# Optimization experiments

Hardware: AMD Instinct MI355X
Metric: run time of the kernel (lower is better)

## Reference

```python
import jax, jax.numpy as jnp
import numpy as np

N, C, D, V, NC = 60000, 4, 200, 5000, 250


def _lin(key, out_d, in_d):
    # torch nn.Linear default init: U(-1/sqrt(in), 1/sqrt(in))
    s = 1.0 / np.sqrt(in_d)
    k1, k2 = jax.random.split(key)
    w = jax.random.uniform(k1, (out_d, in_d), minval=-s, maxval=s, dtype=jnp.float32)
    b = jax.random.uniform(k2, (out_d,), minval=-s, maxval=s, dtype=jnp.float32)
    return w, b


def setup_inputs() -> dict:
    key = jax.random.key(0)
    ks = jax.random.split(key, 16)
    inp = {}
    inp['tokens'] = jax.random.randint(ks[0], (N,), 0, V)
    inp['child_c'] = jax.random.normal(ks[1], (N, C, D), dtype=jnp.float32)
    inp['child_h'] = jax.random.normal(ks[2], (N, C, D), dtype=jnp.float32)
    inp['emb'] = jax.random.normal(ks[3], (V, D), dtype=jnp.float32)
    # ForBlock: proj1: 3D->D, proj2: 2D->D
    inp['p1_w'], inp['p1_b'] = _lin(ks[4], D, 3 * D)
    inp['p2_w'], inp['p2_b'] = _lin(ks[5], D, 2 * D)
    # treelstm gates (each Linear D->D)
    for i, g in enumerate(['ix', 'ih', 'fx', 'fh', 'ux', 'uh', 'ox', 'oh']):
        w, b = _lin(ks[6 + i], D, D)
        inp[g + '_w'], inp[g + '_b'] = w, b
    inp['fc2_w'], inp['fc2_b'] = _lin(ks[14], NC, D)
    return inp


def reference(tokens, child_c, child_h, emb,
              p1_w, p1_b, p2_w, p2_b,
              ix_w, ix_b, ih_w, ih_b, fx_w, fx_b, fh_w, fh_b,
              ux_w, ux_b, uh_w, uh_b, ox_w, ox_b, oh_w, oh_b,
              fc2_w, fc2_b):
    x = emb[tokens]  # [N, D] node token embeddings (nn.Embedding lookup)
    # ForBlock: control = relu(proj1(cat[init, cond, next])); hsum = relu(proj2(cat[control, block]))
    control = jax.nn.relu(
        jnp.concatenate([child_h[:, 0], child_h[:, 1], child_h[:, 2]], axis=-1) @ p1_w.T + p1_b)
    child_h_sum = jax.nn.relu(
        jnp.concatenate([control, child_h[:, 3]], axis=-1) @ p2_w.T + p2_b)  # [N, D]
    # treelstm.node update (vectorized over N nodes, C children)
    i = jax.nn.sigmoid(x @ ix_w.T + ix_b + child_h_sum @ ih_w.T + ih_b)
    o = jax.nn.sigmoid(x @ ox_w.T + ox_b + child_h_sum @ oh_w.T + oh_b)
    u = jnp.tanh(x @ ux_w.T + ux_b + child_h_sum @ uh_w.T + uh_b)
    fx = (x @ fx_w.T + fx_b)[:, None, :]  # [N, 1, D]
    f = jax.nn.sigmoid(jnp.einsum('ncd,md->ncm', child_h, fh_w) + fh_b + fx)  # [N, C, D]
    c = i * u + jnp.sum(f * child_c, axis=1)  # [N, D]
    h = o * jnp.tanh(c)  # [N, D]
    logits = h @ fc2_w.T + fc2_b  # [N, n_class]
    return logits
```

## Files before the change

kernel.cpp:

```cpp
#include <hip/hip_runtime.h>
#include <cmath>

#define NNODES 60000
#define DDIM   200
#define NCLS   250

constexpr int R   = 64;
constexpr int BK  = 32;
constexpr int XP  = 232;

typedef float  f32x4  __attribute__((ext_vector_type(4)));
typedef short  short8 __attribute__((ext_vector_type(8)));

constexpr int W_P1  = 0;
constexpr int W_P2A = 155648;
constexpr int W_P2B = 212992;
constexpr int W_FX  = 270336;
constexpr int W_FH  = 327680;
constexpr int W_IX  = 385024;
constexpr int W_IH  = 442368;
constexpr int W_UX  = 499712;
constexpr int W_UH  = 557056;
constexpr int W_OX  = 614400;
constexpr int W_OH  = 671744;
constexpr int W_FC2 = 729088;
constexpr int W_TOTAL_ELEMS = 786432;
constexpr size_t W_TOTAL_BYTES = (size_t)W_TOTAL_ELEMS * 2;

__device__ __forceinline__ short f2b(float f) {
    union { float f; unsigned u; } x; x.f = f;
    unsigned r = (x.u + 0x7FFFu + ((x.u >> 16) & 1u)) >> 16;
    return (short)r;
}
__device__ __forceinline__ float b2f(short s) {
    union { unsigned u; float f; } x; x.u = ((unsigned)(unsigned short)s) << 16;
    return x.f;
}
__device__ __forceinline__ float sgm(float x)  { return 1.0f / (1.0f + __expf(-x)); }
__device__ __forceinline__ float tanh_fast(float x) { return 1.0f - 2.0f / (__expf(2.0f * x) + 1.0f); }
__device__ __forceinline__ int   swz(int b)    { return b ^ (((b >> 7) & 3) << 4); }

__global__ void wprep(const float* __restrict__ p1w, const float* __restrict__ p2w,
                      const float* __restrict__ fxw, const float* __restrict__ fhw,
                      const float* __restrict__ ixw, const float* __restrict__ ihw,
                      const float* __restrict__ uxw, const float* __restrict__ uhw,
                      const float* __restrict__ oxw, const float* __restrict__ ohw,
                      const float* __restrict__ fc2w, short* __restrict__ ws)
{
    int i = blockIdx.x * 256 + threadIdx.x;
    if (i >= W_TOTAL_ELEMS) return;
    float v = 0.0f;
    if (i < W_P2A) {
        int n = i / 608, k = i % 608;
        if (n < 200 && k < 600) v = p1w[n * 600 + k];
        ws[i] = f2b(v); return;
    }
    int j = i - W_P2A;
    int m = j / 57344, rem = j % 57344;
    int n = rem / 224, k = rem % 224;
    const float* src; int stride = 200, off = 0, ncols = 200;
    switch (m) {
        case 0:  src = p2w; stride = 400; break;
        case 1:  src = p2w; stride = 400; off = 200; break;
        case 2:  src = fxw; break;
        case 3:  src = fhw; break;
        case 4:  src = ixw; break;
        case 5:  src = ihw; break;
        case 6:  src = uxw; break;
        case 7:  src = uhw; break;
        case 8:  src = oxw; break;
        case 9:  src = ohw; break;
        default: src = fc2w; ncols = 250; break;
    }
    if (n < ncols && k < 200) v = src[n * stride + off + k];
    ws[i] = f2b(v);
}

__device__ __forceinline__ void gload16(const void* g, void* l) {
    __builtin_amdgcn_global_load_lds((const __attribute__((address_space(1))) unsigned*)g,
                                     (__attribute__((address_space(3))) unsigned*)l, 16, 0, 0);
}

__device__ __forceinline__ void stage_w(const short* __restrict__ wmat, int Kpad, int t,
                                        int wrows, int wv, short* w_sw)
{
    const int issues = wrows >> 4;
    for (int q = wv; q < issues; q += 4) {
        const int lane = threadIdx.x & 63;
        const int db = q * 1024 + lane * 16;
        const int n  = db >> 6;
        const int g  = (db >> 4) & 3;
        const int gs = g ^ ((n >> 1) & 3);
        const short* src = wmat + (long)n * Kpad + t * BK + gs * 8;
        char* dst = ((char*)w_sw) + q * 1024;
        gload16(src, dst);
    }
}

__device__ __forceinline__ void stage_a_chh(short* a_sw, const float* __restrict__ ag,
                                            int row0, int colofs, int k0, int Kreal, int tid)
{
    const int r = tid >> 2, gq = tid & 3;
    long rg = row0 + r; if (rg >= NNODES) rg = NNODES - 1;
    const float* src = ag + rg * 800 + colofs + k0 + gq * 8;
    short8 v;
    if (k0 + BK <= Kreal) {
        float4 f0 = *(const float4*)(src);
        float4 f1 = *(const float4*)(src + 4);
        v[0] = f2b(f0.x); v[1] = f2b(f0.y); v[2] = f2b(f0.z); v[3] = f2b(f0.w);
        v[4] = f2b(f1.x); v[5] = f2b(f1.y); v[6] = f2b(f1.z); v[7] = f2b(f1.w);
    } else {
        #pragma unroll
        for (int i = 0; i < 8; ++i) {
            int k = k0 + gq * 8 + i;
            float f = (k < Kreal) ? src[i] : 0.0f;
            v[i] = f2b(f);
        }
    }
    int b = r * 64 + gq * 16; b = swz(b);
    *(short8*)((char*)a_sw + b) = v;
}

template<int NF, bool FROM_GLOBAL>
__device__ __forceinline__ void gemm_pass(
    f32x4 (*acc)[8],
    const short (*Ap)[XP],
    const float* __restrict__ ag, int row0, int colofs, int Kreal,
    const short* __restrict__ wmat, int ktiles, int Kpad, int wrows,
    short* a_sw, short* w_sw,
    int tid, int wv, int wm, int wn, int l15, int lg)
{
    for (int t = 0; t < ktiles; ++t) {
        __syncthreads();
        stage_w(wmat, Kpad, t, wrows, wv, w_sw);
        if constexpr (FROM_GLOBAL)
            stage_a_chh(a_sw, ag, row0, colofs, t * BK, Kreal, tid);
        __syncthreads();
        short8 af[2];
        #pragma unroll
        for (int mi = 0; mi < 2; ++mi) {
            const int row = wm * 32 + mi * 16 + l15;
            if constexpr (FROM_GLOBAL) {
                int b = swz(row * 64 + lg * 16);
                af[mi] = *(const short8*)((const char*)a_sw + b);
            } else {
                af[mi] = *(const short8*)&Ap[row][t * BK + lg * 8];
            }
        }
        #pragma unroll
        for (int ni = 0; ni < NF; ++ni) {
            const int n = (wn * NF + ni) * 16 + l15;
            int b = swz(n * 64 + lg * 16);
            short8 bf = *(const short8*)((const char*)w_sw + b);
            #pragma unroll
            for (int mi = 0; mi < 2; ++mi)
                acc[mi][ni] = __builtin_amdgcn_mfma_f32_16x16x32_bf16(af[mi], bf, acc[mi][ni], 0, 0, 0);
        }
    }
}

#define ZERO_ACC()  { _Pragma("unroll") for (int mi_=0; mi_<2; ++mi_) { _Pragma("unroll") for (int ni_=0; ni_<8; ++ni_) { _Pragma("unroll") for (int q_=0;q_<4;++q_) acc[mi_][ni_][q_] = 0.0f; } } }

__global__ __launch_bounds__(256, 2)
void fused_mfma(const int* __restrict__ tok,
                const float* __restrict__ chc,
                const float* __restrict__ chh,
                const float* __restrict__ emb,
                const float* __restrict__ p1b_, const float* __restrict__ p2b_,
                const float* __restrict__ ixb, const float* __restrict__ ihb,
                const float* __restrict__ fxb, const float* __restrict__ fhb,
                const float* __restrict__ uxb, const float* __restrict__ uhb,
                const float* __restrict__ oxb, const float* __restrict__ ohb,
                const float* __restrict__ fc2b,
                const short* __restrict__ ws,
                float* __restrict__ out)
{
    __shared__ __align__(16) short x_lds[R][XP];
    __shared__ __align__(16) short hbuf[R][XP];
    __shared__ __align__(16) short a_sw[R * BK];
    __shared__ __align__(16) short w_sw[8192];

    const int tid = threadIdx.x;
    const int wv = tid >> 6, wm = wv >> 1, wn = wv & 1;
    const int l15 = tid & 15, lg = (tid & 63) >> 4;
    const int row0 = blockIdx.x * R;

    {
        const int r = tid >> 2, q = tid & 3;
        #pragma unroll
        for (int c = 200 + q * 8; c < 200 + q * 8 + 8; ++c) { x_lds[r][c] = 0; hbuf[r][c] = 0; }
        long rg = row0 + r; if (rg >= NNODES) rg = NNODES - 1;
        const float* er = emb + (long)tok[rg] * DDIM;
        const int c0 = q * 50;
        #pragma unroll
        for (int i = 0; i < 50; i += 2) {
            float2 f = *(const float2*)(er + c0 + i);
            x_lds[r][c0 + i]     = f2b(f.x);
            x_lds[r][c0 + i + 1] = f2b(f.y);
        }
    }

    f32x4 acc[2][8];

    ZERO_ACC();
    gemm_pass<7, true>(acc, nullptr, chh, row0, 0, 600, ws + W_P1, 19, 608, 224,
                       a_sw, w_sw, tid, wv, wm, wn, l15, lg);
    #pragma unroll
    for (int mi = 0; mi < 2; ++mi)
        #pragma unroll
        for (int ni = 0; ni < 7; ++ni) {
            const int col = (wn * 7 + ni) * 16 + l15;
            if (col < DDIM) {
                const float b = p1b_[col];
                #pragma unroll
                for (int j = 0; j < 4; ++j) {
                    const int lrow = wm * 32 + mi * 16 + lg * 4 + j;
                    hbuf[lrow][col] = f2b(fmaxf(acc[mi][ni][j] + b, 0.0f));
                }
            }
        }

    ZERO_ACC();
    gemm_pass<7, false>(acc, hbuf, nullptr, 0, 0, 0, ws + W_P2A, 7, 224, 224,
                        a_sw, w_sw, tid, wv, wm, wn, l15, lg);
    gemm_pass<7, true>(acc, nullptr, chh, row0, 600, 200, ws + W_P2B, 7, 224, 224,
                       a_sw, w_sw, tid, wv, wm, wn, l15, lg);
    #pragma unroll
    for (int mi = 0; mi < 2; ++mi)
        #pragma unroll
        for (int ni = 0; ni < 7; ++ni) {
            const int col = (wn * 7 + ni) * 16 + l15;
            if (col < DDIM) {
                const float b = p2b_[col];
                #pragma unroll
                for (int j = 0; j < 4; ++j) {
                    const int lrow = wm * 32 + mi * 16 + lg * 4 + j;
                    hbuf[lrow][col] = f2b(fmaxf(acc[mi][ni][j] + b, 0.0f));
                }
            }
        }

    float giu[2][7][4];
    ZERO_ACC();
    gemm_pass<7, false>(acc, x_lds, nullptr, 0, 0, 0, ws + W_IX, 7, 224, 224,
                        a_sw, w_sw, tid, wv, wm, wn, l15, lg);
    gemm_pass<7, false>(acc, hbuf, nullptr, 0, 0, 0, ws + W_IH, 7, 224, 224,
                        a_sw, w_sw, tid, wv, wm, wn, l15, lg);
    #pragma unroll
    for (int mi = 0; mi < 2; ++mi)
        #pragma unroll
        for (int ni = 0; ni < 7; ++ni) {
            const int col = (wn * 7 + ni) * 16 + l15;
            const float b = (col < DDIM) ? (ixb[col] + ihb[col]) : 0.0f;
            #pragma unroll
            for (int j = 0; j < 4; ++j) giu[mi][ni][j] = sgm(acc[mi][ni][j] + b);
        }

    ZERO_ACC();
    gemm_pass<7, false>(acc, x_lds, nullptr, 0, 0, 0, ws + W_UX, 7, 224, 224,
                        a_sw, w_sw, tid, wv, wm, wn, l15, lg);
    gemm_pass<7, false>(acc, hbuf, nullptr, 0, 0, 0, ws + W_UH, 7, 224, 224,
                        a_sw, w_sw, tid, wv, wm, wn, l15, lg);
    #pragma unroll
    for (int mi = 0; mi < 2; ++mi)
        #pragma unroll
        for (int ni = 0; ni < 7; ++ni) {
            const int col = (wn * 7 + ni) * 16 + l15;
            const float b = (col < DDIM) ? (uxb[col] + uhb[col]) : 0.0f;
            #pragma unroll
            for (int j = 0; j < 4; ++j) giu[mi][ni][j] *= tanh_fast(acc[mi][ni][j] + b);
        }

    ZERO_ACC();
    gemm_pass<7, false>(acc, x_lds, nullptr, 0, 0, 0, ws + W_OX, 7, 224, 224,
                        a_sw, w_sw, tid, wv, wm, wn, l15, lg);
    gemm_pass<7, false>(acc, hbuf, nullptr, 0, 0, 0, ws + W_OH, 7, 224, 224,
                        a_sw, w_sw, tid, wv, wm, wn, l15, lg);
    __syncthreads();
    #pragma unroll
    for (int mi = 0; mi < 2; ++mi)
        #pragma unroll
        for (int ni = 0; ni < 7; ++ni) {
            const int col = (wn * 7 + ni) * 16 + l15;
            if (col < DDIM) {
                const float b = oxb[col] + ohb[col];
                #pragma unroll
                for (int j = 0; j < 4; ++j) {
                    const int lrow = wm * 32 + mi * 16 + lg * 4 + j;
                    hbuf[lrow][col] = f2b(sgm(acc[mi][ni][j] + b));
                }
            }
        }

    float fxr[2][7][4];
    ZERO_ACC();
    gemm_pass<7, false>(acc, x_lds, nullptr, 0, 0, 0, ws + W_FX, 7, 224, 224,
                        a_sw, w_sw, tid, wv, wm, wn, l15, lg);
    #pragma unroll
    for (int mi = 0; mi < 2; ++mi)
        #pragma unroll
        for (int ni = 0; ni < 7; ++ni) {
            const int col = (wn * 7 + ni) * 16 + l15;
            const float b = (col < DDIM) ? fxb[col] : 0.0f;
            #pragma unroll
            for (int j = 0; j < 4; ++j) fxr[mi][ni][j] = acc[mi][ni][j] + b;
        }

    __syncthreads();
    #pragma unroll
    for (int mi = 0; mi < 2; ++mi)
        #pragma unroll
        for (int ni = 0; ni < 7; ++ni) {
            const int col = (wn * 7 + ni) * 16 + l15;
            if (col < DDIM) {
                #pragma unroll
                for (int j = 0; j < 4; ++j) {
                    const int lrow = wm * 32 + mi * 16 + lg * 4 + j;
                    x_lds[lrow][col] = f2b(giu[mi][ni][j]);
                }
            }
        }

    float csum[2][7][4];
    #pragma unroll
    for (int mi = 0; mi < 2; ++mi)
        #pragma unroll
        for (int ni = 0; ni < 7; ++ni)
            #pragma unroll
            for (int j = 0; j < 4; ++j) csum[mi][ni][j] = 0.0f;

    for (int c = 0; c < 4; ++c) {
        ZERO_ACC();
        gemm_pass<7, true>(acc, nullptr, chh, row0, c * 200, 200, ws + W_FH, 7, 224, 224,
                           a_sw, w_sw, tid, wv, wm, wn, l15, lg);
        #pragma unroll
        for (int mi = 0; mi < 2; ++mi)
            #pragma unroll
            for (int ni = 0; ni < 7; ++ni) {
                const int col = (wn * 7 + ni) * 16 + l15;
                if (col < DDIM) {
                    const float b = fhb[col];
                    #pragma unroll
                    for (int j = 0; j < 4; ++j) {
                        const int lrow = wm * 32 + mi * 16 + lg * 4 + j;
                        long rg = row0 + lrow; if (rg >= NNODES) rg = NNODES - 1;
                        const float cv = chc[rg * 800 + c * 200 + col];
                        csum[mi][ni][j] += sgm(acc[mi][ni][j] + b + fxr[mi][ni][j]) * cv;
                    }
                }
            }
    }

    #pragma unroll
    for (int mi = 0; mi < 2; ++mi)
        #pragma unroll
        for (int ni = 0; ni < 7; ++ni) {
            const int col = (wn * 7 + ni) * 16 + l15;
            if (col < DDIM) {
                #pragma unroll
                for (int j = 0; j < 4; ++j) {
                    const int lrow = wm * 32 + mi * 16 + lg * 4 + j;
                    const float iu = b2f(x_lds[lrow][col]);
                    const float o  = b2f(hbuf[lrow][col]);
                    const float cc = iu + csum[mi][ni][j];
                    hbuf[lrow][col] = f2b(o * tanh_fast(cc));
                }
            }
        }

    ZERO_ACC();
    gemm_pass<8, false>(acc, hbuf, nullptr, 0, 0, 0, ws + W_FC2, 7, 224, 256,
                        a_sw, w_sw, tid, wv, wm, wn, l15, lg);
    #pragma unroll
    for (int mi = 0; mi < 2; ++mi)
        #pragma unroll
        for (int ni = 0; ni < 8; ++ni) {
            const int col = (wn * 8 + ni) * 16 + l15;
            if (col < NCLS) {
                const float b = fc2b[col];
                #pragma unroll
                for (int j = 0; j < 4; ++j) {
                    const int lrow = wm * 32 + mi * 16 + lg * 4 + j;
                    const long gr = row0 + lrow;
                    if (gr < NNODES) out[gr * NCLS + col] = acc[mi][ni][j] + b;
                }
            }
        }
}

constexpr int FRT = 32, FBK = 16, FNT = 256, FRTP = FRT + 4, FBUFP = 208;
__device__ __forceinline__ float sgm_f(float x) { return 1.0f / (1.0f + expf(-x)); }

__device__ __forceinline__ void f_stage(
    float (*aT)[FRTP], float (*wt)[FNT], int row0, int k0,
    const float* a1g, int a1pitch, const int* gidx, const float* a1l, int a1lp, int K1,
    const float* a2g, int a2pitch, const float* a2l, int a2lp, int K2,
    const float* wa, int wap, int KW1, const float* wb, int wbp,
    int ncols, int tid)
{
    const int Ktot = K1 + K2;
    {
        const int kk = tid & 15, k = k0 + kk;
        #pragma unroll
        for (int h = 0; h < 2; ++h) {
            const int r = (tid >> 4) + h * 16;
            float v = 0.0f;
            if (k < K1) {
                if (a1l) v = a1l[r * a1lp + k];
                else {
                    const long rb = gidx ? (long)gidx[row0 + r] * a1pitch : (long)(row0 + r) * a1pitch;
                    v = a1g[rb + k];
                }
            } else if (k < Ktot) {
                if (a2l) v = a2l[r * a2lp + (k - K1)];
                else     v = a2g[(long)(row0 + r) * a2pitch + (k - K1)];
            }
            aT[kk][r] = v;
        }
    }
    {
        const int col = tid;
        #pragma unroll
        for (int kk = 0; kk < FBK; ++kk) {
            const int k = k0 + kk; float v = 0.0f;
            if (col < ncols && k < Ktot) {
                if (k < KW1) v = wa[(long)col * wap + k];
                else         v = wb[(long)col * wbp + (k - KW1)];
            }
            wt[kk][col] = v;
        }
    }
}
__device__ __forceinline__ void f_gemm(
    float (*aT)[FRTP], float (*wt)[FNT], float acc[8][4], int row0,
    const float* a1g, int a1p, const int* gidx, const float* a1l, int a1lp, int K1,
    const float* a2g, int a2p, const float* a2l, int a2lp, int K2,
    const float* wa, int wap, int KW1, const float* wb, int wbp,
    int ncols, int tid, int tr, int tc)
{
    #pragma unroll
    for (int j = 0; j < 8; ++j)
        #pragma unroll
        for (int i = 0; i < 4; ++i) acc[j][i] = 0.0f;
    const int Ktot = K1 + K2;
    for (int k0 = 0; k0 < Ktot; k0 += FBK) {
        __syncthreads();
        f_stage(aT, wt, row0, k0, a1g, a1p, gidx, a1l, a1lp, K1, a2g, a2p, a2l, a2lp, K2,
                wa, wap, KW1, wb, wbp, ncols, tid);
        __syncthreads();
        #pragma unroll
        for (int kk = 0; kk < FBK; ++kk) {
            const float w0 = wt[kk][tc*4+0], w1 = wt[kk][tc*4+1], w2 = wt[kk][tc*4+2], w3 = wt[kk][tc*4+3];
            #pragma unroll
            for (int j = 0; j < 8; ++j) {
                const float a = aT[kk][tr*8+j];
                acc[j][0] = fmaf(a, w0, acc[j][0]); acc[j][1] = fmaf(a, w1, acc[j][1]);
                acc[j][2] = fmaf(a, w2, acc[j][2]); acc[j][3] = fmaf(a, w3, acc[j][3]);
            }
        }
    }
}
__global__ __launch_bounds__(256)
void fused_fp32(const int* tok, const float* chc, const float* chh, const float* emb,
                const float* p1w, const float* p1b, const float* p2w, const float* p2b,
                const float* ixw, const float* ixb, const float* ihw, const float* ihb,
                const float* fxw, const float* fxb, const float* fhw, const float* fhb,
                const float* uxw, const float* uxb, const float* uhw, const float* uhb,
                const float* oxw, const float* oxb, const float* ohw, const float* ohb,
                const float* fc2w, const float* fc2b, float* out)
{
    __shared__ float aT[FBK][FRTP]; __shared__ float wt[FBK][FNT]; __shared__ float buf[FRT][FBUFP];
    const int tid = threadIdx.x, tr = tid >> 6, tc = tid & 63, c0 = tc * 4;
    const int row0 = blockIdx.x * FRT;
    float acc[8][4];
    f_gemm(aT, wt, acc, row0, chh, 800, nullptr, nullptr, 0, 600, nullptr,0,nullptr,0,0, p1w,600,600,nullptr,0, DDIM, tid,tr,tc);
    if (c0 < DDIM) { const float4 b = *(const float4*)&p1b[c0];
        #pragma unroll
        for (int j=0;j<8;++j){int r=tr*8+j; buf[r][c0]=fmaxf(acc[j][0]+b.x,0.f); buf[r][c0+1]=fmaxf(acc[j][1]+b.y,0.f); buf[r][c0+2]=fmaxf(acc[j][2]+b.z,0.f); buf[r][c0+3]=fmaxf(acc[j][3]+b.w,0.f);} }
    f_gemm(aT, wt, acc, row0, nullptr,0,nullptr,&buf[0][0],FBUFP,200, chh+600,800,nullptr,0,200, p2w,400,400,nullptr,0, DDIM, tid,tr,tc);
    if (c0 < DDIM) { const float4 b = *(const float4*)&p2b[c0];
        #pragma unroll
        for (int j=0;j<8;++j){int r=tr*8+j; buf[r][c0]=fmaxf(acc[j][0]+b.x,0.f); buf[r][c0+1]=fmaxf(acc[j][1]+b.y,0.f); buf[r][c0+2]=fmaxf(acc[j][2]+b.z,0.f); buf[r][c0+3]=fmaxf(acc[j][3]+b.w,0.f);} }
    f_gemm(aT, wt, acc, row0, emb, DDIM, tok, nullptr,0,200, nullptr,0,nullptr,0,0, fxw,200,200,nullptr,0, DDIM, tid,tr,tc);
    float fxr[8][4];
    { float4 b = make_float4(0,0,0,0); if (c0<DDIM) b = *(const float4*)&fxb[c0];
      #pragma unroll
      for (int j=0;j<8;++j){fxr[j][0]=acc[j][0]+b.x;fxr[j][1]=acc[j][1]+b.y;fxr[j][2]=acc[j][2]+b.z;fxr[j][3]=acc[j][3]+b.w;} }
    float csum[8][4];
    #pragma unroll
    for (int j=0;j<8;++j)
        #pragma unroll
        for (int i=0;i<4;++i) csum[j][i]=0.f;
    for (int cc_=0; cc_<4; ++cc_) {
        f_gemm(aT, wt, acc, row0, chh+cc_*200,800,nullptr,nullptr,0,200, nullptr,0,nullptr,0,0, fhw,200,200,nullptr,0, DDIM, tid,tr,tc);
        if (c0 < DDIM) { const float4 b = *(const float4*)&fhb[c0];
            #pragma unroll
            for (int j=0;j<8;++j){ const long r=row0+tr*8+j; const float4 cv=*(const float4*)&chc[r*800+cc_*200+c0];
                csum[j][0]+=sgm_f(acc[j][0]+b.x+fxr[j][0])*cv.x; csum[j][1]+=sgm_f(acc[j][1]+b.y+fxr[j][1])*cv.y;
                csum[j][2]+=sgm_f(acc[j][2]+b.z+fxr[j][2])*cv.z; csum[j][3]+=sgm_f(acc[j][3]+b.w+fxr[j][3])*cv.w; } }
    }
    f_gemm(aT, wt, acc, row0, emb, DDIM, tok, nullptr,0,200, nullptr,0,&buf[0][0],FBUFP,200, ixw,200,200,ihw,200, DDIM, tid,tr,tc);
    float gi[8][4];
    { float4 b1=make_float4(0,0,0,0),b2=b1; if(c0<DDIM){b1=*(const float4*)&ixb[c0];b2=*(const float4*)&ihb[c0];}
      #pragma unroll
      for(int j=0;j<8;++j){gi[j][0]=sgm_f(acc[j][0]+b1.x+b2.x);gi[j][1]=sgm_f(acc[j][1]+b1.y+b2.y);gi[j][2]=sgm_f(acc[j][2]+b1.z+b2.z);gi[j][3]=sgm_f(acc[j][3]+b1.w+b2.w);} }
    f_gemm(aT, wt, acc, row0, emb, DDIM, tok, nullptr,0,200, nullptr,0,&buf[0][0],FBUFP,200, uxw,200,200,uhw,200, DDIM, tid,tr,tc);
    float cval[8][4];
    { float4 b1=make_float4(0,0,0,0),b2=b1; if(c0<DDIM){b1=*(const float4*)&uxb[c0];b2=*(const float4*)&uhb[c0];}
      #pragma unroll
      for(int j=0;j<8;++j){cval[j][0]=gi[j][0]*tanhf(acc[j][0]+b1.x+b2.x)+csum[j][0];cval[j][1]=gi[j][1]*tanhf(acc[j][1]+b1.y+b2.y)+csum[j][1];
                           cval[j][2]=gi[j][2]*tanhf(acc[j][2]+b1.z+b2.z)+csum[j][2];cval[j][3]=gi[j][3]*tanhf(acc[j][3]+b1.w+b2.w)+csum[j][3];} }
    f_gemm(aT, wt, acc, row0, emb, DDIM, tok, nullptr,0,200, nullptr,0,&buf[0][0],FBUFP,200, oxw,200,200,ohw,200, DDIM, tid,tr,tc);
    if (c0 < DDIM) { const float4 b1=*(const float4*)&oxb[c0], b2=*(const float4*)&ohb[c0];
        #pragma unroll
        for(int j=0;j<8;++j){int r=tr*8+j;
            buf[r][c0]=sgm_f(acc[j][0]+b1.x+b2.x)*tanhf(cval[j][0]); buf[r][c0+1]=sgm_f(acc[j][1]+b1.y+b2.y)*tanhf(cval[j][1]);
            buf[r][c0+2]=sgm_f(acc[j][2]+b1.z+b2.z)*tanhf(cval[j][2]); buf[r][c0+3]=sgm_f(acc[j][3]+b1.w+b2.w)*tanhf(cval[j][3]);} }
    f_gemm(aT, wt, acc, row0, nullptr,0,nullptr,&buf[0][0],FBUFP,200, nullptr,0,nullptr,0,0, fc2w,200,200,nullptr,0, NCLS, tid,tr,tc);
    #pragma unroll
    for (int j=0;j<8;++j){ const long r=row0+tr*8+j;
        #pragma unroll
        for (int i=0;i<4;++i){ const int col=c0+i; if (col<NCLS) out[r*NCLS+col]=acc[j][i]+fc2b[col]; } }
}

extern "C" void kernel_launch(void* const* d_in, const int* in_sizes, int n_in,
                              void* d_out, int out_size, void* d_ws, size_t ws_size,
                              hipStream_t stream)
{
    const int*   tok  = (const int*)  d_in[0];
    const float* chc  = (const float*)d_in[1];
    const float* chh  = (const float*)d_in[2];
    const float* emb  = (const float*)d_in[3];
    const float* p1w  = (const float*)d_in[4];
    const float* p1b  = (const float*)d_in[5];
    const float* p2w  = (const float*)d_in[6];
    const float* p2b  = (const float*)d_in[7];
    const float* ixw  = (const float*)d_in[8];
    const float* ixb  = (const float*)d_in[9];
    const float* ihw  = (const float*)d_in[10];
    const float* ihb  = (const float*)d_in[11];
    const float* fxw  = (const float*)d_in[12];
    const float* fxb  = (const float*)d_in[13];
    const float* fhw  = (const float*)d_in[14];
    const float* fhb  = (const float*)d_in[15];
    const float* uxw  = (const float*)d_in[16];
    const float* uxb  = (const float*)d_in[17];
    const float* uhw  = (const float*)d_in[18];
    const float* uhb  = (const float*)d_in[19];
    const float* oxw  = (const float*)d_in[20];
    const float* oxb  = (const float*)d_in[21];
    const float* ohw  = (const float*)d_in[22];
    const float* ohb  = (const float*)d_in[23];
    const float* fc2w = (const float*)d_in[24];
    const float* fc2b = (const float*)d_in[25];
    float* out = (float*)d_out;

    if (ws_size >= W_TOTAL_BYTES) {
        short* ws = (short*)d_ws;
        hipLaunchKernelGGL(wprep, dim3((W_TOTAL_ELEMS + 255) / 256), dim3(256), 0, stream,
                           p1w, p2w, fxw, fhw, ixw, ihw, uxw, uhw, oxw, ohw, fc2w, ws);
        hipLaunchKernelGGL(fused_mfma, dim3((NNODES + R - 1) / R), dim3(256), 0, stream,
                           tok, chc, chh, emb,
                           p1b, p2b, ixb, ihb, fxb, fhb, uxb, uhb, oxb, ohb, fc2b,
                           ws, out);
    } else {
        hipLaunchKernelGGL(fused_fp32, dim3(NNODES / FRT), dim3(256), 0, stream,
                           tok, chc, chh, emb, p1w, p1b, p2w, p2b,
                           ixw, ixb, ihw, ihb, fxw, fxb, fhw, fhb,
                           uxw, uxb, uhw, uhb, oxw, oxb, ohw, ohb, fc2w, fc2b, out);
    }
}
```

Before: 363.8 us.

## Load MFMA operands directly from global/registers, drop LDS weight staging and per-tile barriers

Replaces the LDS-staged GEMM passes with register-level operand loading. Weights now come straight from global memory (L2-resident bf16) and child_h activations are converted in registers, with a one-tile software prefetch. This removes the two __syncthreads per k-tile. The gates are reordered so fx and the forget-gate sum are computed first, and intermediates are held as packed bf16 in registers using v_cvt_pk_bf16_f32. In exchange, each wave issues more global loads with no cross-wave reuse of weight tiles, and intermediates lose precision by being stored as bf16.

Measured after the change: 507.5 us. +39.5%, slower.

```diff
diff --git a/kernel.cpp b/kernel.cpp
--- a/kernel.cpp
+++ b/kernel.cpp
@@ -5,12 +5,12 @@
 #define DDIM   200
 #define NCLS   250
 
-constexpr int R   = 64;
-constexpr int BK  = 32;
-constexpr int XP  = 232;
-
-typedef float  f32x4  __attribute__((ext_vector_type(4)));
-typedef short  short8 __attribute__((ext_vector_type(8)));
+constexpr int XP = 208;
+constexpr int SH_TOT = 3 * 64 * XP + 64;
+
+typedef float  f32x4   __attribute__((ext_vector_type(4)));
+typedef short  short8  __attribute__((ext_vector_type(8)));
+typedef short  short4v __attribute__((ext_vector_type(4)));
 
 constexpr int W_P1  = 0;
 constexpr int W_P2A = 155648;
@@ -32,13 +32,19 @@
     unsigned r = (x.u + 0x7FFFu + ((x.u >> 16) & 1u)) >> 16;
     return (short)r;
 }
+__device__ __forceinline__ unsigned cvtpk(float lo, float hi) {
+    unsigned r; asm("v_cvt_pk_bf16_f32 %0, %1, %2" : "=v"(r) : "v"(lo), "v"(hi));
+    return r;
+}
+__device__ __forceinline__ short f2b1(float f) { return (short)(cvtpk(f, f) & 0xffffu); }
 __device__ __forceinline__ float b2f(short s) {
     union { unsigned u; float f; } x; x.u = ((unsigned)(unsigned short)s) << 16;
     return x.f;
 }
+__device__ __forceinline__ float b2f_lo(unsigned u) { return b2f((short)(u & 0xffffu)); }
+__device__ __forceinline__ float b2f_hi(unsigned u) { return b2f((short)(u >> 16)); }
 __device__ __forceinline__ float sgm(float x)  { return 1.0f / (1.0f + __expf(-x)); }
 __device__ __forceinline__ float tanh_fast(float x) { return 1.0f - 2.0f / (__expf(2.0f * x) + 1.0f); }
-__device__ __forceinline__ int   swz(int b)    { return b ^ (((b >> 7) & 3) << 4); }
 
 __global__ void wprep(const float* __restrict__ p1w, const float* __restrict__ p2w,
                       const float* __restrict__ fxw, const float* __restrict__ fhw,
@@ -76,135 +82,153 @@
     ws[i] = f2b(v);
 }
 
-__device__ __forceinline__ void gload16(const void* g, void* l) {
-    __builtin_amdgcn_global_load_lds((const __attribute__((address_space(1))) unsigned*)g,
-                                     (__attribute__((address_space(3))) unsigned*)l, 16, 0, 0);
-}
-
-__device__ __forceinline__ void stage_w(const short* __restrict__ wmat, int Kpad, int t,
-                                        int wrows, int wv, short* w_sw)
-{
-    const int issues = wrows >> 4;
-    for (int q = wv; q < issues; q += 4) {
-        const int lane = threadIdx.x & 63;
-        const int db = q * 1024 + lane * 16;
-        const int n  = db >> 6;
-        const int g  = (db >> 4) & 3;
-        const int gs = g ^ ((n >> 1) & 3);
-        const short* src = wmat + (long)n * Kpad + t * BK + gs * 8;
-        char* dst = ((char*)w_sw) + q * 1024;
-        gload16(src, dst);
-    }
-}
-
-__device__ __forceinline__ void stage_a_chh(short* a_sw, const float* __restrict__ ag,
-                                            int row0, int colofs, int k0, int Kreal, int tid)
-{
-    const int r = tid >> 2, gq = tid & 3;
-    long rg = row0 + r; if (rg >= NNODES) rg = NNODES - 1;
-    const float* src = ag + rg * 800 + colofs + k0 + gq * 8;
-    short8 v;
-    if (k0 + BK <= Kreal) {
-        float4 f0 = *(const float4*)(src);
-        float4 f1 = *(const float4*)(src + 4);
-        v[0] = f2b(f0.x); v[1] = f2b(f0.y); v[2] = f2b(f0.z); v[3] = f2b(f0.w);
-        v[4] = f2b(f1.x); v[5] = f2b(f1.y); v[6] = f2b(f1.z); v[7] = f2b(f1.w);
-    } else {
-        #pragma unroll
-        for (int i = 0; i < 8; ++i) {
-            int k = k0 + gq * 8 + i;
-            float f = (k < Kreal) ? src[i] : 0.0f;
-            v[i] = f2b(f);
-        }
-    }
-    int b = r * 64 + gq * 16; b = swz(b);
-    *(short8*)((char*)a_sw + b) = v;
-}
-
-template<int NF, bool FROM_GLOBAL>
-__device__ __forceinline__ void gemm_pass(
-    f32x4 (*acc)[8],
-    const short (*Ap)[XP],
-    const float* __restrict__ ag, int row0, int colofs, int Kreal,
-    const short* __restrict__ wmat, int ktiles, int Kpad, int wrows,
-    short* a_sw, short* w_sw,
-    int tid, int wv, int wm, int wn, int l15, int lg)
-{
-    for (int t = 0; t < ktiles; ++t) {
-        __syncthreads();
-        stage_w(wmat, Kpad, t, wrows, wv, w_sw);
-        if constexpr (FROM_GLOBAL)
-            stage_a_chh(a_sw, ag, row0, colofs, t * BK, Kreal, tid);
-        __syncthreads();
-        short8 af[2];
-        #pragma unroll
-        for (int mi = 0; mi < 2; ++mi) {
-            const int row = wm * 32 + mi * 16 + l15;
-            if constexpr (FROM_GLOBAL) {
-                int b = swz(row * 64 + lg * 16);
-                af[mi] = *(const short8*)((const char*)a_sw + b);
-            } else {
-                af[mi] = *(const short8*)&Ap[row][t * BK + lg * 8];
-            }
-        }
+__device__ __forceinline__ short8 ldw_g(const short* __restrict__ mat, int Kpad, int n, int k) {
+    return *(const short8*)(mat + (long)n * Kpad + k);
+}
+__device__ __forceinline__ short8 lda_g32(const float* __restrict__ p) {
+    float4 f0 = *(const float4*)p;
+    float4 f1 = *(const float4*)(p + 4);
+    unsigned u0 = cvtpk(f0.x, f0.y), u1 = cvtpk(f0.z, f0.w);
+    unsigned u2 = cvtpk(f1.x, f1.y), u3 = cvtpk(f1.z, f1.w);
+    union { unsigned u[4]; short8 s; } c;
+    c.u[0] = u0; c.u[1] = u1; c.u[2] = u2; c.u[3] = u3;
+    return c.s;
+}
+__device__ __forceinline__ short8 lda_l(const short* __restrict__ p) {
+    return *(const short8*)p;
+}
+
+template<int KT>
+__device__ __forceinline__ void pass_ga(f32x4 (&acc)[2][8],
+    const float* __restrict__ a0p, const float* __restrict__ a1p, int Kreal,
+    const short* __restrict__ wp, int Kpad, int nbase, int lg)
+{
+    const int kb = lg * 8;
+    short8 a0 = lda_g32(a0p + kb);
+    short8 a1 = lda_g32(a1p + kb);
+    short8 w[7];
+    #pragma unroll
+    for (int ni = 0; ni < 7; ++ni) w[ni] = ldw_g(wp, Kpad, nbase + ni * 16, kb);
+    #pragma unroll 1
+    for (int t = 0; t < KT; ++t) {
+        const int kn = (t + 1) * 32 + kb;
+        const int ka = (t + 1 < KT) ? ((kn < Kreal) ? kn : 0) : 0;
+        const int kw = (t + 1 < KT) ? kn : 0;
+        short8 na0 = lda_g32(a0p + ka);
+        short8 na1 = lda_g32(a1p + ka);
+        short8 nw[7];
+        #pragma unroll
+        for (int ni = 0; ni < 7; ++ni) nw[ni] = ldw_g(wp, Kpad, nbase + ni * 16, kw);
+        #pragma unroll
+        for (int ni = 0; ni < 7; ++ni) {
+            acc[0][ni] = __builtin_amdgcn_mfma_f32_16x16x32_bf16(a0, w[ni], acc[0][ni], 0, 0, 0);
+            acc[1][ni] = __builtin_amdgcn_mfma_f32_16x16x32_bf16(a1, w[ni], acc[1][ni], 0, 0, 0);
+        }
+        a0 = na0; a1 = na1;
+        #pragma unroll
+        for (int ni = 0; ni < 7; ++ni) w[ni] = nw[ni];
+    }
+}
+
+template<int KT, int NF>
+__device__ __forceinline__ void pass_la(f32x4 (&acc)[2][8],
+    const short* __restrict__ l0, const short* __restrict__ l1,
+    const short* __restrict__ wp, int Kpad, int nbase, int lg)
+{
+    const int kb = lg * 8;
+    short8 a0 = lda_l(l0 + kb);
+    short8 a1 = lda_l(l1 + kb);
+    short8 w[NF];
+    #pragma unroll
+    for (int ni = 0; ni < NF; ++ni) w[ni] = ldw_g(wp, Kpad, nbase + ni * 16, kb);
+    #pragma unroll 1
+    for (int t = 0; t < KT; ++t) {
+        const int kn = (t + 1) * 32 + kb;
+        const int kw = (t + 1 < KT) ? kn : 0;
+        short8 na0 = lda_l(l0 + kw);
+        short8 na1 = lda_l(l1 + kw);
+        short8 nw[NF];
+        #pragma unroll
+        for (int ni = 0; ni < NF; ++ni) nw[ni] = ldw_g(wp, Kpad, nbase + ni * 16, kw);
         #pragma unroll
         for (int ni = 0; ni < NF; ++ni) {
-            const int n = (wn * NF + ni) * 16 + l15;
-            int b = swz(n * 64 + lg * 16);
-            short8 bf = *(const short8*)((const char*)w_sw + b);
-            #pragma unroll
-            for (int mi = 0; mi < 2; ++mi)
-                acc[mi][ni] = __builtin_amdgcn_mfma_f32_16x16x32_bf16(af[mi], bf, acc[mi][ni], 0, 0, 0);
-        }
+            acc[0][ni] = __builtin_amdgcn_mfma_f32_16x16x32_bf16(a0, w[ni], acc[0][ni], 0, 0, 0);
+            acc[1][ni] = __builtin_amdgcn_mfma_f32_16x16x32_bf16(a1, w[ni], acc[1][ni], 0, 0, 0);
+        }
+        a0 = na0; a1 = na1;
+        #pragma unroll
+        for (int ni = 0; ni < NF; ++ni) w[ni] = nw[ni];
     }
 }
 
 #define ZERO_ACC()  { _Pragma("unroll") for (int mi_=0; mi_<2; ++mi_) { _Pragma("unroll") for (int ni_=0; ni_<8; ++ni_) { _Pragma("unroll") for (int q_=0;q_<4;++q_) acc[mi_][ni_][q_] = 0.0f; } } }
 
 __global__ __launch_bounds__(256, 2)
-void fused_mfma(const int* __restrict__ tok,
-                const float* __restrict__ chc,
-                const float* __restrict__ chh,
-                const float* __restrict__ emb,
-                const float* __restrict__ p1b_, const float* __restrict__ p2b_,
-                const float* __restrict__ ixb, const float* __restrict__ ihb,
-                const float* __restrict__ fxb, const float* __restrict__ fhb,
-                const float* __restrict__ uxb, const float* __restrict__ uhb,
-                const float* __restrict__ oxb, const float* __restrict__ ohb,
-                const float* __restrict__ fc2b,
-                const short* __restrict__ ws,
-                float* __restrict__ out)
-{
-    __shared__ __align__(16) short x_lds[R][XP];
-    __shared__ __align__(16) short hbuf[R][XP];
-    __shared__ __align__(16) short a_sw[R * BK];
-    __shared__ __align__(16) short w_sw[8192];
+void fused_v2(const int* __restrict__ tok,
+              const float* __restrict__ chc,
+              const float* __restrict__ chh,
+              const float* __restrict__ emb,
+              const float* __restrict__ p1b_, const float* __restrict__ p2b_,
+              const float* __restrict__ ixb, const float* __restrict__ ihb,
+              const float* __restrict__ fxb, const float* __restrict__ fhb,
+              const float* __restrict__ uxb, const float* __restrict__ uhb,
+              const float* __restrict__ oxb, const float* __restrict__ ohb,
+              const float* __restrict__ fc2b,
+              const short* __restrict__ ws,
+              float* __restrict__ out)
+{
+    __shared__ __align__(16) short SH[SH_TOT];
+    short* bufA = SH;
+    short* bufB = SH + 64 * XP;
+    short* bufX = SH + 2 * 64 * XP;
 
     const int tid = threadIdx.x;
     const int wv = tid >> 6, wm = wv >> 1, wn = wv & 1;
-    const int l15 = tid & 15, lg = (tid & 63) >> 4;
-    const int row0 = blockIdx.x * R;
+    const int l6 = tid & 63, l15 = tid & 15, lg = l6 >> 4;
+    const int row0 = blockIdx.x * 64;
+    const int nb7 = wn * 112 + l15;
+    const int nb8 = wn * 128 + l15;
 
     {
-        const int r = tid >> 2, q = tid & 3;
-        #pragma unroll
-        for (int c = 200 + q * 8; c < 200 + q * 8 + 8; ++c) { x_lds[r][c] = 0; hbuf[r][c] = 0; }
+        short8 z = (short8)0;
+        short8* shv = (short8*)SH;
+        for (int i = tid; i < SH_TOT / 8; i += 256) shv[i] = z;
+    }
+    __syncthreads();
+
+    long rA0 = row0 + wm * 32 + l15;      if (rA0 >= NNODES) rA0 = NNODES - 1;
+    long rA1 = row0 + wm * 32 + 16 + l15; if (rA1 >= NNODES) rA1 = NNODES - 1;
+    const float* chh0 = chh + rA0 * 800;
+    const float* chh1 = chh + rA1 * 800;
+
+    const short* x0 = bufX + (wm * 32 + l15) * XP;
+    const short* x1 = x0 + 16 * XP;
+    const short* hA0 = bufA + (wm * 32 + l15) * XP;
+    const short* hA1 = hA0 + 16 * XP;
+    const short* hB0 = bufB + (wm * 32 + l15) * XP;
+    const short* hB1 = hB0 + 16 * XP;
+
+    {
+        const int r = wm * 32 + (l6 >> 1);
+        const int half = l6 & 1;
         long rg = row0 + r; if (rg >= NNODES) rg = NNODES - 1;
-        const float* er = emb + (long)tok[rg] * DDIM;
-        const int c0 = q * 50;
-        #pragma unroll
-        for (int i = 0; i < 50; i += 2) {
-            float2 f = *(const float2*)(er + c0 + i);
-            x_lds[r][c0 + i]     = f2b(f.x);
-            x_lds[r][c0 + i + 1] = f2b(f.y);
+        const float* er = emb + (long)tok[rg] * DDIM + half * 100;
+        short* xd = bufX + r * XP + half * 100;
+        #pragma unroll 1
+        for (int i = 0; i < 100; i += 4) {
+            float4 f = *(const float4*)(er + i);
+            unsigned u0 = cvtpk(f.x, f.y), u1 = cvtpk(f.z, f.w);
+            short4v s;
+            s[0] = (short)(u0 & 0xffffu); s[1] = (short)(u0 >> 16);
+            s[2] = (short)(u1 & 0xffffu); s[3] = (short)(u1 >> 16);
+            *(short4v*)(xd + i) = s;
         }
     }
 
     f32x4 acc[2][8];
 
     ZERO_ACC();
-    gemm_pass<7, true>(acc, nullptr, chh, row0, 0, 600, ws + W_P1, 19, 608, 224,
-                       a_sw, w_sw, tid, wv, wm, wn, l15, lg);
+    pass_ga<19>(acc, chh0, chh1, 600, ws + W_P1, 608, nb7, lg);
     #pragma unroll
     for (int mi = 0; mi < 2; ++mi)
         #pragma unroll
@@ -214,17 +238,16 @@
                 const float b = p1b_[col];
                 #pragma unroll
                 for (int j = 0; j < 4; ++j) {
-                    const int lrow = wm * 32 + mi * 16 + lg * 4 + j;
-                    hbuf[lrow][col] = f2b(fmaxf(acc[mi][ni][j] + b, 0.0f));
+                    const int lr = wm * 32 + mi * 16 + lg * 4 + j;
+                    bufA[lr * XP + col] = f2b1(fmaxf(acc[mi][ni][j] + b, 0.0f));
                 }
             }
         }
-
-    ZERO_ACC();
-    gemm_pass<7, false>(acc, hbuf, nullptr, 0, 0, 0, ws + W_P2A, 7, 224, 224,
-                        a_sw, w_sw, tid, wv, wm, wn, l15, lg);
-    gemm_pass<7, true>(acc, nullptr, chh, row0, 600, 200, ws + W_P2B, 7, 224, 224,
-                       a_sw, w_sw, tid, wv, wm, wn, l15, lg);
+    __syncthreads();
+
+    ZERO_ACC();
+    pass_la<7, 7>(acc, hA0, hA1, ws + W_P2A, 224, nb7, lg);
+    pass_ga<7>(acc, chh0 + 600, chh1 + 600, 200, ws + W_P2B, 224, nb7, lg);
     #pragma unroll
     for (int mi = 0; mi < 2; ++mi)
         #pragma unroll
@@ -234,33 +257,75 @@
                 const float b = p2b_[col];
                 #pragma unroll
                 for (int j = 0; j < 4; ++j) {
-                    const int lrow = wm * 32 + mi * 16 + lg * 4 + j;
-                    hbuf[lrow][col] = f2b(fmaxf(acc[mi][ni][j] + b, 0.0f));
+                    const int lr = wm * 32 + mi * 16 + lg * 4 + j;
+                    bufB[lr * XP + col] = f2b1(fmaxf(acc[mi][ni][j] + b, 0.0f));
                 }
             }
         }
-
-    float giu[2][7][4];
-    ZERO_ACC();
-    gemm_pass<7, false>(acc, x_lds, nullptr, 0, 0, 0, ws + W_IX, 7, 224, 224,
-                        a_sw, w_sw, tid, wv, wm, wn, l15, lg);
-    gemm_pass<7, false>(acc, hbuf, nullptr, 0, 0, 0, ws + W_IH, 7, 224, 224,
-                        a_sw, w_sw, tid, wv, wm, wn, l15, lg);
+    __syncthreads();
+
+    unsigned fxr_pk[2][7][2];
+    ZERO_ACC();
+    pass_la<7, 7>(acc, x0, x1, ws + W_FX, 224, nb7, lg);
+    #pragma unroll
+    for (int mi = 0; mi < 2; ++mi)
+        #pragma unroll
+        for (int ni = 0; ni < 7; ++ni) {
+            const int col = (wn * 7 + ni) * 16 + l15;
+            const float b = (col < DDIM) ? fxb[col] : 0.0f;
+            fxr_pk[mi][ni][0] = cvtpk(acc[mi][ni][0] + b, acc[mi][ni][1] + b);
+            fxr_pk[mi][ni][1] = cvtpk(acc[mi][ni][2] + b, acc[mi][ni][3] + b);
+        }
+
+    float csum[2][7][4];
+    #pragma unroll
+    for (int mi = 0; mi < 2; ++mi)
+        #pragma unroll
+        for (int ni = 0; ni < 7; ++ni)
+            #pragma unroll
+            for (int j = 0; j < 4; ++j) csum[mi][ni][j] = 0.0f;
+
+    #pragma unroll 1
+    for (int c = 0; c < 4; ++c) {
+        ZERO_ACC();
+        pass_ga<7>(acc, chh0 + c * 200, chh1 + c * 200, 200, ws + W_FH, 224, nb7, lg);
+        #pragma unroll
+        for (int mi = 0; mi < 2; ++mi)
+            #pragma unroll
+            for (int ni = 0; ni < 7; ++ni) {
+                const int col = (wn * 7 + ni) * 16 + l15;
+                if (col < DDIM) {
+                    const float fb = fhb[col];
+                    #pragma unroll
+                    for (int j = 0; j < 4; ++j) {
+                        long rg = row0 + wm * 32 + mi * 16 + lg * 4 + j;
+                        if (rg >= NNODES) rg = NNODES - 1;
+                        const float cv = chc[rg * 800 + c * 200 + col];
+                        const unsigned pk = fxr_pk[mi][ni][j >> 1];
+                        const float fx = (j & 1) ? b2f_hi(pk) : b2f_lo(pk);
+                        csum[mi][ni][j] += sgm(acc[mi][ni][j] + fb + fx) * cv;
+                    }
+                }
+            }
+    }
+
+    unsigned gi_pk[2][7][2];
+    ZERO_ACC();
+    pass_la<7, 7>(acc, x0, x1, ws + W_IX, 224, nb7, lg);
+    pass_la<7, 7>(acc, hB0, hB1, ws + W_IH, 224, nb7, lg);
     #pragma unroll
     for (int mi = 0; mi < 2; ++mi)
         #pragma unroll
         for (int ni = 0; ni < 7; ++ni) {
             const int col = (wn * 7 + ni) * 16 + l15;
             const float b = (col < DDIM) ? (ixb[col] + ihb[col]) : 0.0f;
-            #pragma unroll
-            for (int j = 0; j < 4; ++j) giu[mi][ni][j] = sgm(acc[mi][ni][j] + b);
-        }
-
-    ZERO_ACC();
-    gemm_pass<7, false>(acc, x_lds, nullptr, 0, 0, 0, ws + W_UX, 7, 224, 224,
-                        a_sw, w_sw, tid, wv, wm, wn, l15, lg);
-    gemm_pass<7, false>(acc, hbuf, nullptr, 0, 0, 0, ws + W_UH, 7, 224, 224,
-                        a_sw, w_sw, tid, wv, wm, wn, l15, lg);
+            gi_pk[mi][ni][0] = cvtpk(sgm(acc[mi][ni][0] + b), sgm(acc[mi][ni][1] + b));
+            gi_pk[mi][ni][1] = cvtpk(sgm(acc[mi][ni][2] + b), sgm(acc[mi][ni][3] + b));
+        }
+
+    ZERO_ACC();
+    pass_la<7, 7>(acc, x0, x1, ws + W_UX, 224, nb7, lg);
+    pass_la<7, 7>(acc, hB0, hB1, ws + W_UH, 224, nb7, lg);
     #pragma unroll
     for (int mi = 0; mi < 2; ++mi)
         #pragma unroll
@@ -268,14 +333,16 @@
             const int col = (wn * 7 + ni) * 16 + l15;
             const float b = (col < DDIM) ? (uxb[col] + uhb[col]) : 0.0f;
             #pragma unroll
-            for (int j = 0; j < 4; ++j) giu[mi][ni][j] *= tanh_fast(acc[mi][ni][j] + b);
-        }
-
-    ZERO_ACC();
-    gemm_pass<7, false>(acc, x_lds, nullptr, 0, 0, 0, ws + W_OX, 7, 224, 224,
-                        a_sw, w_sw, tid, wv, wm, wn, l15, lg);
-    gemm_pass<7, false>(acc, hbuf, nullptr, 0, 0, 0, ws + W_OH, 7, 224, 224,
-                        a_sw, w_sw, tid, wv, wm, wn, l15, lg);
+            for (int j = 0; j < 4; ++j) {
+                const unsigned pk = gi_pk[mi][ni][j >> 1];
+                const float gi = (j & 1) ? b2f_hi(pk) : b2f_lo(pk);
+                csum[mi][ni][j] = gi * tanh_fast(acc[mi][ni][j] + b) + csum[mi][ni][j];
+            }
+        }
+
+    ZERO_ACC();
+    pass_la<7, 7>(acc, x0, x1, ws + W_OX, 224, nb7, lg);
+    pass_la<7, 7>(acc, hB0, hB1, ws + W_OH, 224, nb7, lg);
     __syncthreads();
     #pragma unroll
     for (int mi = 0; mi < 2; ++mi)
@@ -286,91 +353,16 @@
                 const float b = oxb[col] + ohb[col];
                 #pragma unroll
                 for (int j = 0; j < 4; ++j) {
-                    const int lrow = wm * 32 + mi * 16 + lg * 4 + j;
-                    hbuf[lrow][col] = f2b(sgm(acc[mi][ni][j] + b));
+                    const int lr = wm * 32 + mi * 16 + lg * 4 + j;
+                    const float h = sgm(acc[mi][ni][j] + b) * tanh_fast(csum[mi][ni][j]);
+                    bufA[lr * XP + col] = f2b1(h);
                 }
             }
         }
-
-    float fxr[2][7][4];
-    ZERO_ACC();
-    gemm_pass<7, false>(acc, x_lds, nullptr, 0, 0, 0, ws + W_FX, 7, 224, 224,
-                        a_sw, w_sw, tid, wv, wm, wn, l15, lg);
-    #pragma unroll
-    for (int mi = 0; mi < 2; ++mi)
-        #pragma unroll
-        for (int ni = 0; ni < 7; ++ni) {
-            const int col = (wn * 7 + ni) * 16 + l15;
-            const float b = (col < DDIM) ? fxb[col] : 0.0f;
-            #pragma unroll
-            for (int j = 0; j < 4; ++j) fxr[mi][ni][j] = acc[mi][ni][j] + b;
-        }
-
     __syncthreads();
-    #pragma unroll
-    for (int mi = 0; mi < 2; ++mi)
-        #pragma unroll
-        for (int ni = 0; ni < 7; ++ni) {
-            const int col = (wn * 7 + ni) * 16 + l15;
-            if (col < DDIM) {
-                #pragma unroll
-                for (int j = 0; j < 4; ++j) {
-                    const int lrow = wm * 32 + mi * 16 + lg * 4 + j;
-                    x_lds[lrow][col] = f2b(giu[mi][ni][j]);
-                }
-            }
-        }
-
-    float csum[2][7][4];
-    #pragma unroll
-    for (int mi = 0; mi < 2; ++mi)
-        #pragma unroll
-        for (int ni = 0; ni < 7; ++ni)
-            #pragma unroll
-            for (int j = 0; j < 4; ++j) csum[mi][ni][j] = 0.0f;
-
-    for (int c = 0; c < 4; ++c) {
-        ZERO_ACC();
-        gemm_pass<7, true>(acc, nullptr, chh, row0, c * 200, 200, ws + W_FH, 7, 224, 224,
-                           a_sw, w_sw, tid, wv, wm, wn, l15, lg);
-        #pragma unroll
-        for (int mi = 0; mi < 2; ++mi)
-            #pragma unroll
-            for (int ni = 0; ni < 7; ++ni) {
-                const int col = (wn * 7 + ni) * 16 + l15;
-                if (col < DDIM) {
-                    const float b = fhb[col];
-                    #pragma unroll
-                    for (int j = 0; j < 4; ++j) {
-                        const int lrow = wm * 32 + mi * 16 + lg * 4 + j;
-                        long rg = row0 + lrow; if (rg >= NNODES) rg = NNODES - 1;
-                        const float cv = chc[rg * 800 + c * 200 + col];
-                        csum[mi][ni][j] += sgm(acc[mi][ni][j] + b + fxr[mi][ni][j]) * cv;
-                    }
-                }
-            }
-    }
-
-    #pragma unroll
-    for (int mi = 0; mi < 2; ++mi)
-        #pragma unroll
-        for (int ni = 0; ni < 7; ++ni) {
-            const int col = (wn * 7 + ni) * 16 + l15;
-            if (col < DDIM) {
-                #pragma unroll
-                for (int j = 0; j < 4; ++j) {
-                    const int lrow = wm * 32 + mi * 16 + lg * 4 + j;
-                    const float iu = b2f(x_lds[lrow][col]);
-                    const float o  = b2f(hbuf[lrow][col]);
-                    const float cc = iu + csum[mi][ni][j];
-                    hbuf[lrow][col] = f2b(o * tanh_fast(cc));
-                }
-            }
-        }
-
-    ZERO_ACC();
-    gemm_pass<8, false>(acc, hbuf, nullptr, 0, 0, 0, ws + W_FC2, 7, 224, 256,
-                        a_sw, w_sw, tid, wv, wm, wn, l15, lg);
+
+    ZERO_ACC();
+    pass_la<7, 8>(acc, hA0, hA1, ws + W_FC2, 224, nb8, lg);
     #pragma unroll
     for (int mi = 0; mi < 2; ++mi)
         #pragma unroll
@@ -380,8 +372,7 @@
                 const float b = fc2b[col];
                 #pragma unroll
                 for (int j = 0; j < 4; ++j) {
-                    const int lrow = wm * 32 + mi * 16 + lg * 4 + j;
-                    const long gr = row0 + lrow;
+                    const long gr = row0 + wm * 32 + mi * 16 + lg * 4 + j;
                     if (gr < NNODES) out[gr * NCLS + col] = acc[mi][ni][j] + b;
                 }
             }
@@ -559,7 +550,7 @@
         short* ws = (short*)d_ws;
         hipLaunchKernelGGL(wprep, dim3((W_TOTAL_ELEMS + 255) / 256), dim3(256), 0, stream,
                            p1w, p2w, fxw, fhw, ixw, ihw, uxw, uhw, oxw, ohw, fc2w, ws);
-        hipLaunchKernelGGL(fused_mfma, dim3((NNODES + R - 1) / R), dim3(256), 0, stream,
+        hipLaunchKernelGGL(fused_v2, dim3((NNODES + 63) / 64), dim3(256), 0, stream,
                            tok, chc, chh, emb,
                            p1b, p2b, ixb, ihb, fxb, fhb, uxb, uhb, oxb, ohb, fc2b,
                            ws, out);
```
